# Optimization experiments

Hardware: AMD Instinct MI355X
Metric: run time of the kernel (lower is better)

The kernel has to match this reference:

```python
import jax, jax.numpy as jnp
import numpy as np

STD = 0.02

def setup_inputs() -> dict:
    key = jax.random.key(0)
    k1, k2, k3 = jax.random.split(key, 3)
    b, n_t, n, n_h = 2, 2048, 256, 8
    r_prime = jax.random.normal(k1, (b, n_t, n), dtype=jnp.float32)
    Q = STD * jax.random.normal(k2, (n_h, n, n), dtype=jnp.float32)
    E = STD * jax.random.normal(k3, (n_h, n, n), dtype=jnp.float32)
    return {"r_prime": r_prime, "Q": Q, "E": E}

def reference(r_prime, Q, E):
    # Omega[b,h,t,u] = sum_ij r'[b,t,i] Q[h,i,j] r'[b,u,j]
    Omega = jnp.einsum('bti,hij,buj->bhtu', r_prime, Q, r_prime)
    n_t = r_prime.shape[1]
    mask = jnp.tril(jnp.ones((n_t, n_t), dtype=r_prime.dtype))  # causal
    Omega = Omega * mask  # broadcast over (b, h)
    # r[b,t,i] = sum_{h,u,j} Omega[b,h,t,u] E[h,i,j] r'[b,u,j]
    r = jnp.einsum('bhtu,hij,buj->bti', Omega, E, r_prime)
    return r
```

## Files before the change

### kernel.cpp

```cpp
#include <hip/hip_runtime.h>
#include <hip/hip_bf16.h>

typedef __bf16 bf16x8 __attribute__((ext_vector_type(8)));
typedef float f32x4 __attribute__((ext_vector_type(4)));
typedef float f32x16 __attribute__((ext_vector_type(16)));

#define NB 2
#define NT 2048
#define ND 256
#define NH 8

__device__ inline __bf16 to_bf16(float f) {
  union { __hip_bfloat16 h; __bf16 b; } u;
  u.h = __float2bfloat16(f);
  return u.b;
}
__device__ inline float bf2f(__bf16 b) {
  union { __bf16 b; unsigned short s; } u; u.b = b;
  union { unsigned int i; float f; } v; v.i = ((unsigned int)u.s) << 16;
  return v.f;
}

typedef __attribute__((address_space(1))) const void g1void;
typedef __attribute__((address_space(3))) void l3void;

__device__ inline void gl_lds16(const void* g, void* l) {
  __builtin_amdgcn_global_load_lds((g1void*)g, (l3void*)l, 16, 0, 0);
}

__device__ inline void stage_tile64_t256(const __bf16* gsrc, __bf16* lds, int tid) {
  const char* wub = (const char*)lds + (tid & ~63) * 16;
#pragma unroll
  for (int p = 0; p < 8; ++p) {
    int lin = p * 256 + tid;
    int row = lin >> 5, c = lin & 31;
    const __bf16* g = gsrc + row * 256 + ((c ^ (row & 31)) << 3);
    gl_lds16((const void*)g, (void*)(wub + p * 4096));
  }
}

__device__ inline void stage_R64(const __bf16* gsrc, __bf16* lds, int w, int lane) {
#pragma unroll
  for (int p = 0; p < 4; ++p) {
    int lin = (p * 8 + w) * 64 + lane;
    int row = lin >> 5, c = lin & 31;
    const __bf16* g = gsrc + row * 256 + ((c ^ (row & 31)) << 3);
    gl_lds16((const void*)g, (void*)((char*)lds + (size_t)(p * 8 + w) * 1024));
  }
}
__device__ inline void stage_V64(const __bf16* gsrc, __bf16* lds, int w, int lane) {
#pragma unroll
  for (int p = 0; p < 4; ++p) {
    int lin = (p * 8 + w) * 64 + lane;
    int row = lin >> 3, c = lin & 7;
    const __bf16* g = gsrc + (size_t)row * NT + ((c ^ (row & 7)) << 3);
    gl_lds16((const void*)g, (void*)((char*)lds + (size_t)(p * 8 + w) * 1024));
  }
}

__global__ __launch_bounds__(256) void convert_kernel(
    const float* __restrict__ r, const float* __restrict__ E,
    __bf16* __restrict__ Rb, __bf16* __restrict__ Eb) {
  int idx = blockIdx.x * blockDim.x + threadIdx.x;
  const int nR = NB * NT * ND;
  const int nQ = NH * ND * ND;
  for (; idx < nR + nQ; idx += gridDim.x * blockDim.x) {
    if (idx < nR) Rb[idx] = to_bf16(r[idx]);
    else Eb[idx - nR] = to_bf16(E[idx - nR]);
  }
}

__global__ __launch_bounds__(256) void transpose_q(
    const float* __restrict__ Q, __bf16* __restrict__ Qt) {
  __shared__ float T[32][33];
  int h = blockIdx.z;
  int i0 = blockIdx.y * 32, j0 = blockIdx.x * 32;
  int r = threadIdx.x >> 3, c4 = (threadIdx.x & 7) * 4;
  f32x4 v = *(const f32x4*)(Q + h * 65536 + (i0 + r) * 256 + j0 + c4);
#pragma unroll
  for (int j = 0; j < 4; ++j) T[r][c4 + j] = v[j];
  __syncthreads();
  __bf16* dst = Qt + h * 65536 + (j0 + r) * 256 + i0 + c4;
#pragma unroll
  for (int j = 0; j < 4; ++j) dst[j] = to_bf16(T[c4 + j][r]);
}

__global__ __launch_bounds__(256, 4) void gemm_stage1(
    const __bf16* __restrict__ Rb, const __bf16* __restrict__ Qt,
    const __bf16* __restrict__ Eb, __bf16* __restrict__ Am,
    __bf16* __restrict__ Vt) {
  __shared__ __bf16 Bs[64 * 256];
  int z = blockIdx.z, x = blockIdx.x;
  const __bf16 *A, *B;
  __bf16* C;
  int m0, n0, cstride;
  if (z < 16) {
    int bb = z >> 3, h = z & 7;
    A = Rb + (size_t)bb * NT * ND;
    B = Qt + (size_t)h * ND * ND;
    C = Am + (size_t)z * NT * ND;
    m0 = (x & 31) * 64; n0 = (x >> 5) * 64; cstride = ND;
  } else {
    int zz = z - 16;
    int bb = zz >> 3, h = zz & 7;
    A = Eb + (size_t)h * ND * ND;
    B = Rb + (size_t)bb * NT * ND;
    C = Vt + (size_t)zz * ND * NT;
    m0 = (x & 3) * 64; n0 = (x >> 2) * 64; cstride = NT;
  }

  int tid = threadIdx.x;
  int lane = tid & 63, w = tid >> 6;
  int l15 = lane & 15, lg = lane >> 4;

  stage_tile64_t256(B + (size_t)n0 * 256, Bs, tid);

  bf16x8 af[8];
  const __bf16* arow = A + (size_t)(m0 + w * 16 + l15) * 256 + lg * 8;
#pragma unroll
  for (int ks = 0; ks < 8; ++ks) af[ks] = *(const bf16x8*)(arow + ks * 32);

  __syncthreads();

  f32x4 acc[4] = {};
#pragma unroll
  for (int ks = 0; ks < 8; ++ks) {
#pragma unroll
    for (int nt = 0; nt < 4; ++nt) {
      int row = nt * 16 + l15;
      int ch = (ks * 4 + lg) ^ (row & 31);
      bf16x8 bfr = *(const bf16x8*)(&Bs[row * 256 + ch * 8]);
      acc[nt] = __builtin_amdgcn_mfma_f32_16x16x32_bf16(af[ks], bfr, acc[nt], 0, 0, 0);
    }
  }
#pragma unroll
  for (int nt = 0; nt < 4; ++nt)
#pragma unroll
    for (int m = 0; m < 4; ++m)
      C[(size_t)(m0 + w * 16 + lg * 4 + m) * cstride + n0 + nt * 16 + l15] =
          to_bf16(acc[nt][m]);
}

__global__ __launch_bounds__(512, 2) void attn_kernel(
    const __bf16* __restrict__ Am, const __bf16* __restrict__ Rb,
    const __bf16* __restrict__ Vt, __bf16* __restrict__ partial,
    float* __restrict__ out, int use_partial) {
  __shared__ __bf16 Rk[2][64 * 256];
  __shared__ __bf16 Vk[2][256 * 64];
  __shared__ __bf16 Sl[128 * 64];

  int xx = blockIdx.x & 7, kk = blockIdx.x >> 3;
  int z = xx + 8 * (kk & 1);
  int local = kk >> 1;
  int px = local >> 1, q = local & 1;
  int b = z >> 3, h = z & 7;

  const __bf16* Amat = Am + (size_t)z * NT * ND;
  const __bf16* R = Rb + (size_t)b * NT * ND;
  const __bf16* V = Vt + (size_t)z * ND * NT;

  int tid = threadIdx.x;
  int w = tid >> 6, lane = tid & 63;
  int l31 = lane & 31, l5 = lane >> 5;
  int swt = w >> 1, swu = w & 1;

#pragma unroll 1
  for (int half = 0; half < 2; ++half) {
    int tt = half ? (15 - px) : px;
    int t0 = tt * 128;
    int ulast = 2 * tt + 1;

    stage_R64(R + (size_t)q * 64 * 256, &Rk[0][0], w, lane);
    stage_V64(V + q * 64, &Vk[0][0], w, lane);

    bf16x8 af[16];
    {
      const __bf16* arow = Amat + (size_t)(t0 + swt * 32 + l31) * ND + l5 * 8;
#pragma unroll
      for (int ks = 0; ks < 16; ++ks) af[ks] = *(const bf16x8*)(arow + ks * 16);
    }

    f32x16 acc[4] = {};

    asm volatile("s_waitcnt vmcnt(0)" ::: "memory");
    __builtin_amdgcn_s_barrier();

    int buf = 0;
#pragma unroll 1
    for (int ut = q; ut <= ulast; ut += 2) {
      int u0 = ut * 64;
      if (ut + 2 <= ulast) {
        stage_R64(R + (size_t)(ut + 2) * 64 * 256, &Rk[buf ^ 1][0], w, lane);
        stage_V64(V + (ut + 2) * 64, &Vk[buf ^ 1][0], w, lane);
      }

      const __bf16* Rcur = &Rk[buf][0];
      int bbase = (swu * 32 + l31) * 256;
      f32x16 s0 = {}, s1 = {};
#pragma unroll
      for (int ks = 0; ks < 8; ++ks) {
        bf16x8 bfr = *(const bf16x8*)(Rcur + bbase + (((ks * 2 + l5) ^ l31) << 3));
        s0 = __builtin_amdgcn_mfma_f32_32x32x16_bf16(af[ks], bfr, s0, 0, 0, 0);
      }
#pragma unroll
      for (int ks = 8; ks < 16; ++ks) {
        bf16x8 bfr = *(const bf16x8*)(Rcur + bbase + (((ks * 2 + l5) ^ l31) << 3));
        s1 = __builtin_amdgcn_mfma_f32_32x32x16_bf16(af[ks], bfr, s1, 0, 0, 0);
      }
      f32x16 s = s0 + s1;

      int ucol = u0 + swu * 32 + l31;
      int cg = swu * 4 + (l31 >> 3);
#pragma unroll
      for (int rg = 0; rg < 16; ++rg) {
        int trow = (rg & 3) + 8 * (rg >> 2) + 4 * l5;
        int srow = swt * 32 + trow;
        float v = (ucol <= t0 + srow) ? s[rg] : 0.0f;
        Sl[srow * 64 + ((cg ^ (srow & 7)) << 3) + (l31 & 7)] = to_bf16(v);
      }
      asm volatile("s_waitcnt lgkmcnt(0)" ::: "memory");
      __builtin_amdgcn_s_barrier();

      bf16x8 sf[4];
      int srow2 = swt * 32 + l31;
#pragma unroll
      for (int ks = 0; ks < 4; ++ks) {
        int c = (ks * 2 + l5) ^ (srow2 & 7);
        sf[ks] = *(const bf16x8*)(Sl + srow2 * 64 + c * 8);
      }
      const __bf16* Vcur = &Vk[buf][0];
#pragma unroll
      for (int it = 0; it < 4; ++it) {
        int irow = swu * 128 + it * 32 + l31;
#pragma unroll
        for (int ks = 0; ks < 4; ++ks) {
          int c = (ks * 2 + l5) ^ (irow & 7);
          bf16x8 vf = *(const bf16x8*)(Vcur + irow * 64 + c * 8);
          acc[it] = __builtin_amdgcn_mfma_f32_32x32x16_bf16(sf[ks], vf, acc[it], 0, 0, 0);
        }
      }
      asm volatile("s_waitcnt vmcnt(0) lgkmcnt(0)" ::: "memory");
      __builtin_amdgcn_s_barrier();
      buf ^= 1;
    }

    __syncthreads();
    __bf16* Ep = &Rk[0][0];
#pragma unroll
    for (int it = 0; it < 4; ++it)
#pragma unroll
      for (int rg = 0; rg < 16; ++rg) {
        int trow = (rg & 3) + 8 * (rg >> 2) + 4 * l5;
        Ep[(swt * 32 + trow) * 256 + swu * 128 + it * 32 + l31] = to_bf16(acc[it][rg]);
      }
    __syncthreads();
    if (use_partial) {
      __bf16* Pdst = partial + ((size_t)(q * NH + h) * NB + b) * NT * ND +
                     (size_t)t0 * ND;
#pragma unroll
      for (int c = 0; c < 8; ++c) {
        int off = c * 512 + tid;
        *(bf16x8*)(Pdst + off * 8) = *(const bf16x8*)(Ep + off * 8);
      }
    } else {
      float* O = out + (size_t)b * NT * ND + (size_t)t0 * ND;
#pragma unroll
      for (int c = 0; c < 8; ++c) {
        int off = c * 512 + tid;
        bf16x8 vv = *(const bf16x8*)(Ep + off * 8);
#pragma unroll
        for (int e = 0; e < 8; ++e) atomicAdd(&O[off * 8 + e], bf2f(vv[e]));
      }
    }
    __syncthreads();
  }
}

__global__ __launch_bounds__(256) void reduce_kernel(
    const __bf16* __restrict__ partial, float* __restrict__ out) {
  size_t gid = (size_t)blockIdx.x * 256 + threadIdx.x;
  size_t e = gid * 8;
  int bb = (int)(e >> 19);
  size_t x = e & ((1u << 19) - 1);
  float sum[8] = {};
#pragma unroll
  for (int s = 0; s < 16; ++s) {
    bf16x8 v = *(const bf16x8*)(partial + (((size_t)(s * NB + bb)) << 19) + x);
#pragma unroll
    for (int j = 0; j < 8; ++j) sum[j] += bf2f(v[j]);
  }
  f32x4 lo = {sum[0], sum[1], sum[2], sum[3]};
  f32x4 hi = {sum[4], sum[5], sum[6], sum[7]};
  *(f32x4*)(out + e) = lo;
  *(f32x4*)(out + e + 4) = hi;
}

extern "C" void kernel_launch(void* const* d_in, const int* in_sizes, int n_in,
                              void* d_out, int out_size, void* d_ws, size_t ws_size,
                              hipStream_t stream) {
  const float* r = (const float*)d_in[0];
  const float* Q = (const float*)d_in[1];
  const float* E = (const float*)d_in[2];
  float* out = (float*)d_out;

  char* ws = (char*)d_ws;
  __bf16* Rb = (__bf16*)(ws);
  __bf16* Qt = (__bf16*)(ws + (2u << 20));
  __bf16* Eb = (__bf16*)(ws + (3u << 20));
  __bf16* Am = (__bf16*)(ws + (4u << 20));
  __bf16* Vt = (__bf16*)(ws + (20u << 20));
  __bf16* Pq = (__bf16*)(ws + (36u << 20));
  int use_partial = (ws_size >= (72ull << 20)) ? 1 : 0;

  if (!use_partial)
    hipMemsetAsync(d_out, 0, (size_t)out_size * sizeof(float), stream);

  convert_kernel<<<1024, 256, 0, stream>>>(r, E, Rb, Eb);
  transpose_q<<<dim3(8, 8, 8), 256, 0, stream>>>(Q, Qt);

  gemm_stage1<<<dim3(128, 1, 32), 256, 0, stream>>>(Rb, Qt, Eb, Am, Vt);

  attn_kernel<<<dim3(256), 512, 0, stream>>>(Am, Rb, Vt, Pq, out, use_partial);

  if (use_partial) reduce_kernel<<<512, 256, 0, stream>>>(Pq, out);
}
```

Before: 150.3 us.

## Merge prep kernels and relax vmcnt waits to overlap staging loads

Combines the fp32-to-bf16 convert and Q transpose kernels into a single launch, removing one kernel launch gap. In the attention kernel, the A-fragment global loads are issued before the LDS staging loads, and the full vmcnt(0) waits are replaced with partial counts so the prefetch of the next R/V tile can stay in flight across barriers. The partial waits assume exact counts of outstanding vector memory ops, so any change in how the compiler emits loads could make them unsafe.

```diff
diff --git a/kernel.cpp b/kernel.cpp
--- a/kernel.cpp
+++ b/kernel.cpp
@@ -58,31 +58,32 @@
   }
 }
 
-__global__ __launch_bounds__(256) void convert_kernel(
-    const float* __restrict__ r, const float* __restrict__ E,
-    __bf16* __restrict__ Rb, __bf16* __restrict__ Eb) {
-  int idx = blockIdx.x * blockDim.x + threadIdx.x;
-  const int nR = NB * NT * ND;
-  const int nQ = NH * ND * ND;
-  for (; idx < nR + nQ; idx += gridDim.x * blockDim.x) {
-    if (idx < nR) Rb[idx] = to_bf16(r[idx]);
-    else Eb[idx - nR] = to_bf16(E[idx - nR]);
-  }
-}
-
-__global__ __launch_bounds__(256) void transpose_q(
-    const float* __restrict__ Q, __bf16* __restrict__ Qt) {
+__global__ __launch_bounds__(256) void prep_kernel(
+    const float* __restrict__ r, const float* __restrict__ Q,
+    const float* __restrict__ E, __bf16* __restrict__ Rb,
+    __bf16* __restrict__ Qt, __bf16* __restrict__ Eb) {
   __shared__ float T[32][33];
-  int h = blockIdx.z;
-  int i0 = blockIdx.y * 32, j0 = blockIdx.x * 32;
-  int r = threadIdx.x >> 3, c4 = (threadIdx.x & 7) * 4;
-  f32x4 v = *(const f32x4*)(Q + h * 65536 + (i0 + r) * 256 + j0 + c4);
-#pragma unroll
-  for (int j = 0; j < 4; ++j) T[r][c4 + j] = v[j];
-  __syncthreads();
-  __bf16* dst = Qt + h * 65536 + (j0 + r) * 256 + i0 + c4;
-#pragma unroll
-  for (int j = 0; j < 4; ++j) dst[j] = to_bf16(T[c4 + j][r]);
+  int bx = blockIdx.x;
+  if (bx < 512) {
+    int h = bx >> 6, i0 = ((bx >> 3) & 7) * 32, j0 = (bx & 7) * 32;
+    int rr = threadIdx.x >> 3, c4 = (threadIdx.x & 7) * 4;
+    f32x4 v = *(const f32x4*)(Q + h * 65536 + (i0 + rr) * 256 + j0 + c4);
+#pragma unroll
+    for (int j = 0; j < 4; ++j) T[rr][c4 + j] = v[j];
+    __syncthreads();
+    __bf16* dst = Qt + h * 65536 + (j0 + rr) * 256 + i0 + c4;
+#pragma unroll
+    for (int j = 0; j < 4; ++j) dst[j] = to_bf16(T[c4 + j][rr]);
+  } else {
+    int idx = (bx - 512) * 256 + threadIdx.x;
+    const int nR = NB * NT * ND;
+    const int nQ = NH * ND * ND;
+    const int stride = 1024 * 256;
+    for (; idx < nR + nQ; idx += stride) {
+      if (idx < nR) Rb[idx] = to_bf16(r[idx]);
+      else Eb[idx - nR] = to_bf16(E[idx - nR]);
+    }
+  }
 }
 
 __global__ __launch_bounds__(256, 4) void gemm_stage1(
@@ -170,26 +171,26 @@
     int t0 = tt * 128;
     int ulast = 2 * tt + 1;
 
-    stage_R64(R + (size_t)q * 64 * 256, &Rk[0][0], w, lane);
-    stage_V64(V + q * 64, &Vk[0][0], w, lane);
-
     bf16x8 af[16];
     {
       const __bf16* arow = Amat + (size_t)(t0 + swt * 32 + l31) * ND + l5 * 8;
 #pragma unroll
       for (int ks = 0; ks < 16; ++ks) af[ks] = *(const bf16x8*)(arow + ks * 16);
     }
+    stage_R64(R + (size_t)q * 64 * 256, &Rk[0][0], w, lane);
+    stage_V64(V + q * 64, &Vk[0][0], w, lane);
 
     f32x16 acc[4] = {};
 
-    asm volatile("s_waitcnt vmcnt(0)" ::: "memory");
+    asm volatile("s_waitcnt vmcnt(4)" ::: "memory");
     __builtin_amdgcn_s_barrier();
 
     int buf = 0;
 #pragma unroll 1
     for (int ut = q; ut <= ulast; ut += 2) {
       int u0 = ut * 64;
-      if (ut + 2 <= ulast) {
+      bool has_next = (ut + 2 <= ulast);
+      if (has_next) {
         stage_R64(R + (size_t)(ut + 2) * 64 * 256, &Rk[buf ^ 1][0], w, lane);
         stage_V64(V + (ut + 2) * 64, &Vk[buf ^ 1][0], w, lane);
       }
@@ -219,6 +220,8 @@
         Sl[srow * 64 + ((cg ^ (srow & 7)) << 3) + (l31 & 7)] = to_bf16(v);
       }
       asm volatile("s_waitcnt lgkmcnt(0)" ::: "memory");
+      if (has_next) asm volatile("s_waitcnt vmcnt(8)" ::: "memory");
+      else          asm volatile("s_waitcnt vmcnt(0)" ::: "memory");
       __builtin_amdgcn_s_barrier();
 
       bf16x8 sf[4];
@@ -239,7 +242,8 @@
           acc[it] = __builtin_amdgcn_mfma_f32_32x32x16_bf16(sf[ks], vf, acc[it], 0, 0, 0);
         }
       }
-      asm volatile("s_waitcnt vmcnt(0) lgkmcnt(0)" ::: "memory");
+      if (has_next) asm volatile("s_waitcnt vmcnt(4)" ::: "memory");
+      else          asm volatile("s_waitcnt vmcnt(0)" ::: "memory");
       __builtin_amdgcn_s_barrier();
       buf ^= 1;
     }
@@ -315,8 +319,7 @@
   if (!use_partial)
     hipMemsetAsync(d_out, 0, (size_t)out_size * sizeof(float), stream);
 
-  convert_kernel<<<1024, 256, 0, stream>>>(r, E, Rb, Eb);
-  transpose_q<<<dim3(8, 8, 8), 256, 0, stream>>>(Q, Qt);
+  prep_kernel<<<1536, 256, 0, stream>>>(r, Q, E, Rb, Qt, Eb);
 
   gemm_stage1<<<dim3(128, 1, 32), 256, 0, stream>>>(Rb, Qt, Eb, Am, Vt);
 
```

Measured after the change: 150.7 us. About the same (+0.3%).
